# Kernel tuning notes

Measured on AMD Instinct MI355X. Metric: run time of the kernel, lower is better.

Reference implementation:

```python
import jax, jax.numpy as jnp
import numpy as np


def _bilinear_resize(x, out_h, out_w):
    """PyTorch-style bilinear resize, align_corners=False, no antialias. x: [B,C,H,W]."""
    B, C, H, W = x.shape
    sy = H / out_h
    sx = W / out_w
    ys = jnp.maximum((jnp.arange(out_h, dtype=x.dtype) + 0.5) * sy - 0.5, 0.0)
    xs = jnp.maximum((jnp.arange(out_w, dtype=x.dtype) + 0.5) * sx - 0.5, 0.0)
    y0 = jnp.minimum(jnp.floor(ys).astype(jnp.int32), H - 1)
    x0 = jnp.minimum(jnp.floor(xs).astype(jnp.int32), W - 1)
    y1 = jnp.minimum(y0 + 1, H - 1)
    x1 = jnp.minimum(x0 + 1, W - 1)
    ty = ys - y0.astype(x.dtype)  # [out_h]
    tx = xs - x0.astype(x.dtype)  # [out_w]
    row = x[:, :, y0, :] * (1.0 - ty)[None, None, :, None] + x[:, :, y1, :] * ty[None, None, :, None]
    out = row[:, :, :, x0] * (1.0 - tx)[None, None, None, :] + row[:, :, :, x1] * tx[None, None, None, :]
    return out


def setup_inputs() -> dict:
    key = jax.random.key(0)
    ks = jax.random.split(key, 6)
    T, B, Ck, Cv = 4, 4, 128, 512
    H, W, h, w = 64, 64, 32, 32
    return {
        "memory_keys": jax.random.normal(ks[0], (T, B, Ck, H, W), dtype=jnp.float32),
        "memory_values": jax.random.normal(ks[1], (T, B, Cv, H, W), dtype=jnp.float32),
        "query_value": jax.random.normal(ks[2], (B, Cv, H, W), dtype=jnp.float32),
        "memory_keys_low": jax.random.normal(ks[3], (T, B, Ck, h, w), dtype=jnp.float32),
        "memory_values_low": jax.random.normal(ks[4], (T, B, Cv, h, w), dtype=jnp.float32),
        "query_key_low": jax.random.normal(ks[5], (B, Ck, h, w), dtype=jnp.float32),
    }


def reference(memory_keys, memory_values, query_value, memory_keys_low, memory_values_low, query_key_low):
    matmul_norm = False  # init default
    T, B, Ck, h, w = memory_keys_low.shape
    H, W = memory_keys.shape[-2:]
    Cv = memory_values.shape[2]

    # ---- low-level memory read ----
    # memory_keys_low -> [B, Ck, T*h*w]
    mkl = jnp.transpose(memory_keys_low.reshape(T, B, Ck, h * w), (1, 2, 0, 3)).reshape(B, Ck, T * h * w)
    qkl = query_key_low.reshape(B, Ck, h * w)
    # key_attention: [B, T*h*w, h*w]
    key_attention = jnp.einsum('bkm,bkq->bmq', mkl, qkl)
    if matmul_norm:
        key_attention = key_attention * (Ck ** -0.5)
    key_attention = jax.nn.softmax(key_attention, axis=1)
    mvl = jnp.transpose(memory_values_low.reshape(T, B, Cv, h * w), (1, 2, 0, 3)).reshape(B, Cv, T * h * w)
    memory = jnp.einsum('bvm,bmq->bvq', mvl, key_attention).reshape(B, Cv, h, w)

    # ---- high-level channel attention ----
    g_keys = jnp.transpose(memory_keys, (1, 0, 2, 3, 4)).reshape(B, T, Ck, H * W)
    g_vals = jnp.transpose(memory_values, (1, 0, 2, 3, 4)).reshape(B, T, Cv, H * W)
    # g_attn: [B, T, Ck, Cv] = keys @ values^T over spatial dim
    g_attn = jnp.einsum('btkp,btvp->btkv', g_keys, g_vals)
    if matmul_norm:
        g_attn = g_attn * (Cv ** -0.5)
    g_attn = jax.nn.softmax(g_attn, axis=1)  # softmax over the T (frame) axis

    qv = query_value.reshape(B, Cv, H * W)
    # [B, T, Ck, H*W] -> [B, T*Ck, H, W]
    qv_out = jnp.einsum('btkv,bvq->btkq', g_attn, qv).reshape(B, T * Ck, H, W)
    qv_out = _bilinear_resize(qv_out, h, w)

    return jnp.concatenate([qv_out, memory], axis=1)  # [B, T*Ck+Cv, h, w]
```

## Files before the change

### kernel.cpp

```cpp
#include <hip/hip_runtime.h>

#define T_ 4
#define B_ 4
#define CK 128
#define CV 512
#define PP 4096
#define QQ 1024
#define MM 4096
#define NS 8

using f32x2  = __attribute__((ext_vector_type(2))) float;
using f32x4  = __attribute__((ext_vector_type(4))) float;
using bf16   = __bf16;
using bf16x2 = __attribute__((ext_vector_type(2))) __bf16;
using bf16x4 = __attribute__((ext_vector_type(4))) __bf16;
using bf16x8 = __attribute__((ext_vector_type(8))) __bf16;
using f16    = _Float16;
using f16x8  = __attribute__((ext_vector_type(8))) _Float16;

__device__ __forceinline__ f32x4 mfma16(bf16x8 a, bf16x8 b, f32x4 c) {
    return __builtin_amdgcn_mfma_f32_16x16x32_bf16(a, b, c, 0, 0, 0);
}
__device__ __forceinline__ f32x4 mfma16h(f16x8 a, f16x8 b, f32x4 c) {
    return __builtin_amdgcn_mfma_f32_16x16x32_f16(a, b, c, 0, 0, 0);
}

__device__ __forceinline__ void gload16(const void* g, void* l) {
    __builtin_amdgcn_global_load_lds(
        (const __attribute__((address_space(1))) void*)g,
        (__attribute__((address_space(3))) void*)l, 16, 0, 0);
}

__global__ __launch_bounds__(256) void k_stage1(
        const float* __restrict__ mkl, const float* __restrict__ qkl,
        bf16* __restrict__ Pt, float* __restrict__ cs_part,
        const float* __restrict__ mvl, bf16* __restrict__ Ab,
        const float* __restrict__ qv,  float* __restrict__ qvp,
        const float* __restrict__ mk,  f16* __restrict__ mkh,
        const float* __restrict__ mv,  f16* __restrict__ mvh) {
    __shared__ __align__(16) char smem[20480];
    const int bid = blockIdx.x;
    const int tid = threadIdx.x;

    if (bid % 3 == 0) {
        bf16* As = (bf16*)smem;
        bf16* Bs = (bf16*)(smem + 10240);
        bf16* Th = (bf16*)smem;

        int lb  = bid / 3;
        int sw  = (lb & 7) * 128 + (lb >> 3);
        const int b  = sw >> 8;
        const int r  = sw & 255;
        const int qy = r >> 5;
        const int mx = r & 31;
        const int m0 = mx * 128;
        const int q0 = qy * 128;
        const int t  = m0 >> 10;
        const int sm0 = m0 & 1023;

        const int lane = tid & 63;
        const int wid  = tid >> 6;
        const int wr = wid >> 1, wc = wid & 1;
        const int g = lane >> 4, li = lane & 15;

        const float* Abase = mkl + (((size_t)(t * B_ + b) * CK) << 10) + sm0;
        const float* Bbase = qkl + (((size_t)b * CK) << 10) + q0;
        const int ml   = tid & 127;
        const int half = tid >> 7;

        const f32x4 fz = {0.f, 0.f, 0.f, 0.f};
        f32x4 acc[4][4];
#pragma unroll
        for (int i = 0; i < 4; ++i)
#pragma unroll
            for (int j = 0; j < 4; ++j) acc[i][j] = fz;

        for (int k0 = 0; k0 < CK; k0 += 32) {
#pragma unroll
            for (int j = 0; j < 8; ++j) {
                int kk = 4 * j + 2 * half;
                float a0 = Abase[(k0 + kk) * 1024 + ml];
                float a1 = Abase[(k0 + kk + 1) * 1024 + ml];
                bf16x2 pa; pa.x = (bf16)a0; pa.y = (bf16)a1;
                *(bf16x2*)(As + ml * 40 + kk) = pa;
                float b0 = Bbase[(k0 + kk) * 1024 + ml];
                float b1 = Bbase[(k0 + kk + 1) * 1024 + ml];
                bf16x2 pb; pb.x = (bf16)b0; pb.y = (bf16)b1;
                *(bf16x2*)(Bs + ml * 40 + kk) = pb;
            }
            __syncthreads();
            bf16x8 af[4], bfr[4];
#pragma unroll
            for (int mf = 0; mf < 4; ++mf)
                af[mf] = *(const bf16x8*)(As + (wr * 64 + mf * 16 + li) * 40 + g * 8);
#pragma unroll
            for (int nf = 0; nf < 4; ++nf)
                bfr[nf] = *(const bf16x8*)(Bs + (wc * 64 + nf * 16 + li) * 40 + g * 8);
#pragma unroll
            for (int mf = 0; mf < 4; ++mf)
#pragma unroll
                for (int nf = 0; nf < 4; ++nf)
                    acc[mf][nf] = mfma16(af[mf], bfr[nf], acc[mf][nf]);
            __syncthreads();
        }

        float cs[4] = {0.f, 0.f, 0.f, 0.f};
        bf16x4 ebuf[4][4];
#pragma unroll
        for (int mf = 0; mf < 4; ++mf)
#pragma unroll
            for (int nf = 0; nf < 4; ++nf) {
                f32x4 v = acc[mf][nf];
                float e0 = __expf(v.x), e1 = __expf(v.y);
                float e2 = __expf(v.z), e3 = __expf(v.w);
                cs[nf] += e0 + e1 + e2 + e3;
                bf16x4 e; e.x = (bf16)e0; e.y = (bf16)e1; e.z = (bf16)e2; e.w = (bf16)e3;
                ebuf[mf][nf] = e;
            }
#pragma unroll
        for (int nf = 0; nf < 4; ++nf) {
            float s = cs[nf];
            s += __shfl_xor(s, 16);
            s += __shfl_xor(s, 32);
            if (g == 0)
                cs_part[(size_t)(((b * 32 + mx) * 2 + wr) << 10) + q0 + wc * 64 + nf * 16 + li] = s;
        }
#pragma unroll
        for (int p = 0; p < 2; ++p) {
            __syncthreads();
            if (wr == p) {
#pragma unroll
                for (int mf = 0; mf < 4; ++mf)
#pragma unroll
                    for (int nf = 0; nf < 4; ++nf) {
                        int col  = wc * 64 + nf * 16 + li;
                        int rowb = mf * 16 + g * 4;
                        *(bf16x4*)(Th + col * 72 + rowb) = ebuf[mf][nf];
                    }
            }
            __syncthreads();
#pragma unroll
            for (int pass = 0; pass < 4; ++pass) {
                int idx = pass * 256 + tid;
                int row = idx >> 3;
                int ch  = (idx & 7) * 8;
                bf16x8 v = *(const bf16x8*)(Th + row * 72 + ch);
                *(bf16x8*)(Pt + (size_t)(b * QQ + q0 + row) * MM + m0 + p * 64 + ch) = v;
            }
        }
    } else {
        int sid = bid - bid / 3 - 1;
        if (sid < 1024) {
            int base = sid * 4096 + tid;
#pragma unroll
            for (int i = 0; i < 16; ++i) {
                int idx = base + i * 256;
                f32x4 a = __builtin_nontemporal_load((const f32x4*)mv + (size_t)idx * 2);
                f32x4 c = __builtin_nontemporal_load((const f32x4*)mv + (size_t)idx * 2 + 1);
                f16x8 o;
                o[0] = (f16)a.x; o[1] = (f16)a.y; o[2] = (f16)a.z; o[3] = (f16)a.w;
                o[4] = (f16)c.x; o[5] = (f16)c.y; o[6] = (f16)c.z; o[7] = (f16)c.w;
                ((f16x8*)mvh)[idx] = o;
            }
        } else if (sid < 1280) {
            int base = (sid - 1024) * 4096 + tid;
#pragma unroll
            for (int i = 0; i < 16; ++i) {
                int idx = base + i * 256;
                f32x4 a = __builtin_nontemporal_load((const f32x4*)mk + (size_t)idx * 2);
                f32x4 c = __builtin_nontemporal_load((const f32x4*)mk + (size_t)idx * 2 + 1);
                f16x8 o;
                o[0] = (f16)a.x; o[1] = (f16)a.y; o[2] = (f16)a.z; o[3] = (f16)a.w;
                o[4] = (f16)c.x; o[5] = (f16)c.y; o[6] = (f16)c.z; o[7] = (f16)c.w;
                ((f16x8*)mkh)[idx] = o;
            }
        } else if (sid < 1536) {
            int base = (sid - 1280) * 4096 + tid;
#pragma unroll
            for (int i = 0; i < 16; ++i) {
                int idx = base + i * 256;
                f32x4 a = __builtin_nontemporal_load((const f32x4*)mvl + (size_t)idx * 2);
                f32x4 c = __builtin_nontemporal_load((const f32x4*)mvl + (size_t)idx * 2 + 1);
                bf16x8 o;
                o[0] = (bf16)a.x; o[1] = (bf16)a.y; o[2] = (bf16)a.z; o[3] = (bf16)a.w;
                o[4] = (bf16)c.x; o[5] = (bf16)c.y; o[6] = (bf16)c.z; o[7] = (bf16)c.w;
                ((bf16x8*)Ab)[idx] = o;
            }
        } else {
            int base = (sid - 1536) * 4096 + tid;
#pragma unroll
            for (int i = 0; i < 16; ++i) {
                int idx = base + i * 256;
                int q  = idx & (QQ - 1);
                int bv = idx >> 10;
                int y = q >> 5, x = q & 31;
                const float* src = qv + ((size_t)bv << 12);
                f32x2 r0 = __builtin_nontemporal_load((const f32x2*)(src + y * 128 + 2 * x));
                f32x2 r1 = __builtin_nontemporal_load((const f32x2*)(src + y * 128 + 64 + 2 * x));
                qvp[idx] = 0.25f * (r0.x + r0.y + r1.x + r1.y);
            }
        }
    }
}

__global__ __launch_bounds__(256, 2) void k_stage2(
        const f16* __restrict__ mkh, const f16* __restrict__ mvh,
        float* __restrict__ Gp,
        const bf16* __restrict__ Ab, const bf16* __restrict__ Pt,
        float* __restrict__ Mp,
        const float* __restrict__ cs_part, float* __restrict__ colsum) {
    __shared__ __align__(16) char smem[65536];
    const int bid = blockIdx.x;
    const int tid = threadIdx.x;

    if (bid < 512) {
        f16* lsA = (f16*)smem;
        f16* lsB = (f16*)(smem + 32768);

        int sw  = (bid & 7) * 64 + (bid >> 3);
        const int bt = sw >> 5;
        const int rx = sw & 31;
        const int ks = rx >> 2;
        const int v0 = (rx & 3) * 128;
        const int b = bt >> 2, t = bt & 3;

        const int lane = tid & 63;
        const int w    = tid >> 6;
        const int wr = w >> 1, wc = w & 1;
        const int g = lane >> 4, li = lane & 15;
        const int rr = lane >> 3;
        const int cg = (lane & 7) ^ rr;

        const f16* Abase = mkh + ((size_t)(t * B_ + b) * CK) * PP + ks * 512;
        const f16* Bbase = mvh + ((size_t)((t * B_ + b) * CV + v0)) * PP + ks * 512;

        auto STAGE = [&](int buf, int j) {
            int mg = j * 64;
#pragma unroll
            for (int cc = 0; cc < 4; ++cc) {
                int c = cc * 4 + w;
                int r = c * 8 + rr;
                gload16(Abase + (size_t)r * PP + mg + cg * 8, lsA + buf * 8192 + c * 512);
                gload16(Bbase + (size_t)r * PP + mg + cg * 8, lsB + buf * 8192 + c * 512);
            }
        };
        auto FRAG = [&](const f16* base, int r, int G) -> f16x8 {
            int x = r & 7;
            return *(const f16x8*)(base + (r >> 3) * 512 + x * 64 + ((G ^ x) * 8));
        };

        const f32x4 fz = {0.f, 0.f, 0.f, 0.f};
        f32x4 acc[4][4];
#pragma unroll
        for (int i = 0; i < 4; ++i)
#pragma unroll
            for (int j = 0; j < 4; ++j) acc[i][j] = fz;

        STAGE(0, 0);
        __syncthreads();
        int cur = 0;

        for (int j = 0; j < 8; ++j) {
            if (j + 1 < 8) STAGE(cur ^ 1, j + 1);
#pragma unroll
            for (int kc = 0; kc < 2; ++kc) {
                f16x8 af[4], bfr[4];
#pragma unroll
                for (int mf = 0; mf < 4; ++mf)
                    af[mf] = FRAG(lsA + cur * 8192, wr * 64 + mf * 16 + li, kc * 4 + g);
#pragma unroll
                for (int nf = 0; nf < 4; ++nf)
                    bfr[nf] = FRAG(lsB + cur * 8192, wc * 64 + nf * 16 + li, kc * 4 + g);
#pragma unroll
                for (int mf = 0; mf < 4; ++mf)
#pragma unroll
                    for (int nf = 0; nf < 4; ++nf)
                        acc[mf][nf] = mfma16h(af[mf], bfr[nf], acc[mf][nf]);
            }
            __syncthreads();
            cur ^= 1;
        }

        float* outp = Gp + (size_t)(ks * 16 + bt) * CK * CV + v0;
#pragma unroll
        for (int mf = 0; mf < 4; ++mf)
#pragma unroll
            for (int nf = 0; nf < 4; ++nf) {
                int k = wr * 64 + mf * 16 + g * 4;
                int v = wc * 64 + nf * 16 + li;
                f32x4 a = acc[mf][nf];
                outp[(size_t)(k + 0) * CV + v] = a.x;
                outp[(size_t)(k + 1) * CV + v] = a.y;
                outp[(size_t)(k + 2) * CV + v] = a.z;
                outp[(size_t)(k + 3) * CV + v] = a.w;
            }
    } else if (bid < 1024) {
        bf16* lsA = (bf16*)smem;
        bf16* lsB = (bf16*)(smem + 32768);

        int mb = bid - 512;
        int sw  = (mb & 7) * 64 + (mb >> 3);
        const int bt = sw >> 5;
        const int rx = sw & 31;
        const int q0 = (rx >> 2) * 128;
        const int v0 = (rx & 3) * 128;
        const int b = bt >> 2, t = bt & 3;

        const int lane = tid & 63;
        const int w    = tid >> 6;
        const int wr = w >> 1, wc = w & 1;
        const int g = lane >> 4, li = lane & 15;
        const int rr = lane >> 3;
        const int cg = (lane & 7) ^ rr;

        const bf16* Abase = Ab + (((size_t)((t * B_ + b) * CV + v0)) << 10);
        const bf16* Bbase = Pt + (size_t)(b * QQ + q0) * MM + t * 1024;

        auto STAGE = [&](int buf, int j) {
            int mg = j * 64;
#pragma unroll
            for (int cc = 0; cc < 4; ++cc) {
                int c = cc * 4 + w;
                int r = c * 8 + rr;
                gload16(Abase + (size_t)r * 1024 + mg + cg * 8, lsA + buf * 8192 + c * 512);
                gload16(Bbase + (size_t)r * MM   + mg + cg * 8, lsB + buf * 8192 + c * 512);
            }
        };
        auto FRAG = [&](const bf16* base, int r, int G) -> bf16x8 {
            int x = r & 7;
            return *(const bf16x8*)(base + (r >> 3) * 512 + x * 64 + ((G ^ x) * 8));
        };

        const f32x4 fz = {0.f, 0.f, 0.f, 0.f};
        f32x4 acc[4][4];
#pragma unroll
        for (int i = 0; i < 4; ++i)
#pragma unroll
            for (int j = 0; j < 4; ++j) acc[i][j] = fz;

        STAGE(0, 0);
        __syncthreads();
        int cur = 0;

        for (int j = 0; j < 16; ++j) {
            if (j + 1 < 16) STAGE(cur ^ 1, j + 1);
#pragma unroll
            for (int kc = 0; kc < 2; ++kc) {
                bf16x8 af[4], bfr[4];
#pragma unroll
                for (int mf = 0; mf < 4; ++mf)
                    af[mf] = FRAG(lsA + cur * 8192, wr * 64 + mf * 16 + li, kc * 4 + g);
#pragma unroll
                for (int nf = 0; nf < 4; ++nf)
                    bfr[nf] = FRAG(lsB + cur * 8192, wc * 64 + nf * 16 + li, kc * 4 + g);
#pragma unroll
                for (int mf = 0; mf < 4; ++mf)
#pragma unroll
                    for (int nf = 0; nf < 4; ++nf)
                        acc[mf][nf] = mfma16(af[mf], bfr[nf], acc[mf][nf]);
            }
            __syncthreads();
            cur ^= 1;
        }

#pragma unroll
        for (int nf = 0; nf < 4; ++nf) {
            int q = q0 + wc * 64 + nf * 16 + li;
#pragma unroll
            for (int mf = 0; mf < 4; ++mf) {
                int v = v0 + wr * 64 + mf * 16 + g * 4;
                f32x4 a = acc[mf][nf];
                float* base = Mp + (((size_t)bt * CV + v) << 10) + q;
                base[0 << 10] = a.x;
                base[1 << 10] = a.y;
                base[2 << 10] = a.z;
                base[3 << 10] = a.w;
            }
        }
    } else {
        int idx = (bid - 1024) * 256 + tid;
        int q = idx & (QQ - 1);
        int b = idx >> 10;
        float s = 0.f;
#pragma unroll 8
        for (int r = 0; r < 64; ++r)
            s += cs_part[(size_t)(((b * 64 + r)) << 10) + q];
        colsum[idx] = s;
    }
}

__global__ __launch_bounds__(256) void k_stage3(
        const float* __restrict__ Gp, bf16* __restrict__ Wt,
        const float* __restrict__ Mp, const float* __restrict__ colsum,
        float* __restrict__ out) {
    const int bid = blockIdx.x;
    const int tid = threadIdx.x;

    if (bid < 1024) {
        int idx = bid * 256 + tid;
        int v = idx & (CV - 1);
        int bk = idx >> 9;
        int k = bk & (CK - 1);
        int b = bk >> 7;
        float gv[4];
#pragma unroll
        for (int t = 0; t < 4; ++t) {
            float s = 0.f;
#pragma unroll
            for (int ks = 0; ks < NS; ++ks)
                s += Gp[((size_t)(ks * 16 + b * 4 + t) * CK + k) * CV + v];
            gv[t] = s;
        }
        float mx = fmaxf(fmaxf(gv[0], gv[1]), fmaxf(gv[2], gv[3]));
        float e[4], sum = 0.f;
#pragma unroll
        for (int t = 0; t < 4; ++t) { e[t] = __expf(gv[t] - mx); sum += e[t]; }
        float inv = 1.f / sum;
#pragma unroll
        for (int t = 0; t < 4; ++t)
            Wt[((size_t)((b * 4 + t) * CK + k)) * CV + v] = (bf16)(e[t] * inv);
    } else {
        int idx = ((bid - 1024) * 256 + tid) * 4;
        int q = idx & (QQ - 1);
        int v = (idx >> 10) & (CV - 1);
        int b = idx >> 19;
        f32x4 s = {0.f, 0.f, 0.f, 0.f};
#pragma unroll
        for (int t = 0; t < 4; ++t) {
            f32x4 m = *(const f32x4*)(Mp + (((size_t)((b * 4 + t) * CV + v)) << 10) + q);
            s.x += m.x; s.y += m.y; s.z += m.z; s.w += m.w;
        }
        f32x4 cs = *(const f32x4*)(colsum + (b << 10) + q);
        f32x4 o;
        o.x = s.x / cs.x; o.y = s.y / cs.y; o.z = s.z / cs.z; o.w = s.w / cs.w;
        *(f32x4*)(out + (((size_t)(b * 1024 + 512 + v)) << 10) + q) = o;
    }
}

__global__ __launch_bounds__(256) void k_qvout(const bf16* __restrict__ Wt,
                                               const float* __restrict__ QVp,
                                               float* __restrict__ out) {
    __shared__ __align__(16) char smem[27648];
    bf16* As = (bf16*)smem;
    bf16* Bs = (bf16*)(smem + 18432);

    int bid = blockIdx.x;
    int sw  = (bid & 7) * 32 + (bid >> 3);
    const int bt = sw >> 4;
    const int q0 = (sw & 15) * 64;
    const int b = bt >> 2, t = bt & 3;

    const int tid = threadIdx.x;
    const int lane = tid & 63;
    const int wid = tid >> 6;
    const int wr = wid >> 1, wc = wid & 1;
    const int g = lane >> 4, li = lane & 15;

    const bf16*  Abase = Wt + (size_t)bt * CK * CV;
    const float* Bbase = QVp + (((size_t)b * CV) << 10) + q0;

    const f32x4 fz = {0.f, 0.f, 0.f, 0.f};
    f32x4 acc[4][2];
#pragma unroll
    for (int i = 0; i < 4; ++i)
#pragma unroll
        for (int j = 0; j < 2; ++j) acc[i][j] = fz;

    const int ql  = tid & 63;
    const int grp = tid >> 6;

    for (int kk = 0; kk < 8; ++kk) {
        int vk0 = kk * 64;
#pragma unroll
        for (int pass = 0; pass < 4; ++pass) {
            int idx = pass * 256 + tid;
            int row = idx >> 3;
            int ch  = (idx & 7) * 8;
            bf16x8 v = *(const bf16x8*)(Abase + (size_t)row * CV + vk0 + ch);
            *(bf16x8*)(As + row * 72 + ch) = v;
        }
#pragma unroll
        for (int j = 0; j < 8; ++j) {
            int vv = 2 * grp + 8 * j;
            float b0 = Bbase[(size_t)(vk0 + vv) * 1024 + ql];
            float b1 = Bbase[(size_t)(vk0 + vv + 1) * 1024 + ql];
            bf16x2 p; p.x = (bf16)b0; p.y = (bf16)b1;
            *(bf16x2*)(Bs + ql * 72 + vv) = p;
        }
        __syncthreads();
#pragma unroll
        for (int kc = 0; kc < 2; ++kc) {
            bf16x8 af[4], bfr[2];
#pragma unroll
            for (int mf = 0; mf < 4; ++mf)
                af[mf] = *(const bf16x8*)(As + (wr * 64 + mf * 16 + li) * 72 + kc * 32 + g * 8);
#pragma unroll
            for (int nf = 0; nf < 2; ++nf)
                bfr[nf] = *(const bf16x8*)(Bs + (wc * 32 + nf * 16 + li) * 72 + kc * 32 + g * 8);
#pragma unroll
            for (int mf = 0; mf < 4; ++mf)
#pragma unroll
                for (int nf = 0; nf < 2; ++nf)
                    acc[mf][nf] = mfma16(af[mf], bfr[nf], acc[mf][nf]);
        }
        __syncthreads();
    }

#pragma unroll
    for (int mf = 0; mf < 4; ++mf)
#pragma unroll
        for (int nf = 0; nf < 2; ++nf) {
            int k = wr * 64 + mf * 16 + g * 4;
            int q = q0 + wc * 32 + nf * 16 + li;
            f32x4 a = acc[mf][nf];
            size_t base = ((size_t)(b * 1024 + t * 128 + k) << 10) + q;
            out[base]             = a.x;
            out[base + (1 << 10)] = a.y;
            out[base + (2 << 10)] = a.z;
            out[base + (3 << 10)] = a.w;
        }
}

extern "C" void kernel_launch(void* const* d_in, const int* in_sizes, int n_in,
                              void* d_out, int out_size, void* d_ws, size_t ws_size,
                              hipStream_t stream) {
    (void)in_sizes; (void)n_in; (void)out_size; (void)ws_size;
    const float* mk  = (const float*)d_in[0];
    const float* mv  = (const float*)d_in[1];
    const float* qv  = (const float*)d_in[2];
    const float* mkl = (const float*)d_in[3];
    const float* mvl = (const float*)d_in[4];
    const float* qkl = (const float*)d_in[5];
    float* out = (float*)d_out;

    char* w = (char*)d_ws;
    bf16*  Pt      = (bf16*)w;  w += (size_t)B_ * QQ * MM * 2;
    float* QVp     = (float*)w; w += (size_t)B_ * CV * QQ * 4;
    float* Gp      = (float*)w; w += (size_t)NS * 16 * CK * CV * 4;
    bf16*  Wt      = (bf16*)w;  w += (size_t)B_ * T_ * CK * CV * 2;
    float* colsum  = (float*)w; w += (size_t)B_ * QQ * 4;
    bf16*  Ab      = (bf16*)w;  w += (size_t)T_ * B_ * CV * QQ * 2;
    float* cs_part = (float*)w; w += (size_t)B_ * 64 * QQ * 4;
    float* Mp      = (float*)w; w += (size_t)T_ * B_ * CV * QQ * 4;
    f16*   mkh     = (f16*)w;   w += (size_t)T_ * B_ * CK * PP * 2;
    f16*   mvh     = (f16*)w;   w += (size_t)T_ * B_ * CV * PP * 2;

    k_stage1<<<dim3(3072), 256, 0, stream>>>(mkl, qkl, Pt, cs_part,
                                             mvl, Ab, qv, QVp,
                                             mk, mkh, mv, mvh);
    k_stage2<<<dim3(1040), 256, 0, stream>>>(mkh, mvh, Gp, Ab, Pt, Mp,
                                             cs_part, colsum);
    k_stage3<<<dim3(3072), 256, 0, stream>>>(Gp, Wt, Mp, colsum, out);
    k_qvout <<<dim3(256),  256, 0, stream>>>(Wt, QVp, out);
}
```

Measured before the change: 137.5 us.

## Accumulate memory-read partials atomically into output and halve channel-attention K splits

The per-frame memory-read partial buffer Mp is removed. Stage 2 now atomically adds its per-T partial products straight into the zeroed output region, and stage 3 reads and normalises them in place, which drops a large intermediate write and read. The channel-attention GEMM split count goes from 8 to 4, with longer K loops per block, so less partial data goes to Gp, and its blocks are interleaved with the memory-read blocks. Stage 1 also zeroes the output slice and vectorises the qv downsample. The cost is float atomics, which make the summation order nondeterministic and may contend, plus fewer blocks for the GEMM.

```diff
diff --git a/kernel.cpp b/kernel.cpp
--- a/kernel.cpp
+++ b/kernel.cpp
@@ -7,7 +7,7 @@
 #define PP 4096
 #define QQ 1024
 #define MM 4096
-#define NS 8
+#define NS 4
 
 using f32x2  = __attribute__((ext_vector_type(2))) float;
 using f32x4  = __attribute__((ext_vector_type(4))) float;
@@ -37,7 +37,8 @@
         const float* __restrict__ mvl, bf16* __restrict__ Ab,
         const float* __restrict__ qv,  float* __restrict__ qvp,
         const float* __restrict__ mk,  f16* __restrict__ mkh,
-        const float* __restrict__ mv,  f16* __restrict__ mvh) {
+        const float* __restrict__ mv,  f16* __restrict__ mvh,
+        float* __restrict__ out) {
     __shared__ __align__(16) char smem[20480];
     const int bid = blockIdx.x;
     const int tid = threadIdx.x;
@@ -186,18 +187,31 @@
                 o[4] = (bf16)c.x; o[5] = (bf16)c.y; o[6] = (bf16)c.z; o[7] = (bf16)c.w;
                 ((bf16x8*)Ab)[idx] = o;
             }
-        } else {
+        } else if (sid < 1792) {
             int base = (sid - 1536) * 4096 + tid;
 #pragma unroll
             for (int i = 0; i < 16; ++i) {
-                int idx = base + i * 256;
-                int q  = idx & (QQ - 1);
-                int bv = idx >> 10;
-                int y = q >> 5, x = q & 31;
-                const float* src = qv + ((size_t)bv << 12);
-                f32x2 r0 = __builtin_nontemporal_load((const f32x2*)(src + y * 128 + 2 * x));
-                f32x2 r1 = __builtin_nontemporal_load((const f32x2*)(src + y * 128 + 64 + 2 * x));
-                qvp[idx] = 0.25f * (r0.x + r0.y + r1.x + r1.y);
+                int pidx = base + i * 256;
+                int pr = pidx & 511;
+                int bv = pidx >> 9;
+                int y = pr >> 4, xp = pr & 15;
+                const float* src = qv + ((size_t)bv << 12) + y * 128 + xp * 4;
+                f32x4 r0 = __builtin_nontemporal_load((const f32x4*)src);
+                f32x4 r1 = __builtin_nontemporal_load((const f32x4*)(src + 64));
+                f32x2 o;
+                o.x = 0.25f * (r0.x + r0.y + r1.x + r1.y);
+                o.y = 0.25f * (r0.z + r0.w + r1.z + r1.w);
+                *(f32x2*)(qvp + ((size_t)bv << 10) + y * 32 + xp * 2) = o;
+            }
+        } else if (sid < 1856) {
+            int base = (sid - 1792) * 8192 + tid;
+            const f32x4 z = {0.f, 0.f, 0.f, 0.f};
+#pragma unroll
+            for (int i = 0; i < 32; ++i) {
+                int zidx = base + i * 256;
+                int b   = zidx >> 17;
+                int off = zidx & 131071;
+                ((f32x4*)out)[(size_t)b * 262144 + 131072 + off] = z;
             }
         }
     }
@@ -207,19 +221,20 @@
         const f16* __restrict__ mkh, const f16* __restrict__ mvh,
         float* __restrict__ Gp,
         const bf16* __restrict__ Ab, const bf16* __restrict__ Pt,
-        float* __restrict__ Mp,
+        float* __restrict__ out,
         const float* __restrict__ cs_part, float* __restrict__ colsum) {
     __shared__ __align__(16) char smem[65536];
     const int bid = blockIdx.x;
     const int tid = threadIdx.x;
 
-    if (bid < 512) {
+    if (bid < 768 && bid % 3 == 0) {
         f16* lsA = (f16*)smem;
         f16* lsB = (f16*)(smem + 32768);
 
-        int sw  = (bid & 7) * 64 + (bid >> 3);
-        const int bt = sw >> 5;
-        const int rx = sw & 31;
+        int gid = bid / 3;
+        int sw  = (gid & 7) * 32 + (gid >> 3);
+        const int bt = sw >> 4;
+        const int rx = sw & 15;
         const int ks = rx >> 2;
         const int v0 = (rx & 3) * 128;
         const int b = bt >> 2, t = bt & 3;
@@ -231,8 +246,8 @@
         const int rr = lane >> 3;
         const int cg = (lane & 7) ^ rr;
 
-        const f16* Abase = mkh + ((size_t)(t * B_ + b) * CK) * PP + ks * 512;
-        const f16* Bbase = mvh + ((size_t)((t * B_ + b) * CV + v0)) * PP + ks * 512;
+        const f16* Abase = mkh + ((size_t)(t * B_ + b) * CK) * PP + ks * 1024;
+        const f16* Bbase = mvh + ((size_t)((t * B_ + b) * CV + v0)) * PP + ks * 1024;
 
         auto STAGE = [&](int buf, int j) {
             int mg = j * 64;
@@ -260,8 +275,8 @@
         __syncthreads();
         int cur = 0;
 
-        for (int j = 0; j < 8; ++j) {
-            if (j + 1 < 8) STAGE(cur ^ 1, j + 1);
+        for (int j = 0; j < 16; ++j) {
+            if (j + 1 < 16) STAGE(cur ^ 1, j + 1);
 #pragma unroll
             for (int kc = 0; kc < 2; ++kc) {
                 f16x8 af[4], bfr[4];
@@ -294,11 +309,11 @@
                 outp[(size_t)(k + 2) * CV + v] = a.z;
                 outp[(size_t)(k + 3) * CV + v] = a.w;
             }
-    } else if (bid < 1024) {
+    } else if (bid < 768) {
         bf16* lsA = (bf16*)smem;
         bf16* lsB = (bf16*)(smem + 32768);
 
-        int mb = bid - 512;
+        int mb = bid - bid / 3 - 1;
         int sw  = (mb & 7) * 64 + (mb >> 3);
         const int bt = sw >> 5;
         const int rx = sw & 31;
@@ -370,15 +385,15 @@
             for (int mf = 0; mf < 4; ++mf) {
                 int v = v0 + wr * 64 + mf * 16 + g * 4;
                 f32x4 a = acc[mf][nf];
-                float* base = Mp + (((size_t)bt * CV + v) << 10) + q;
-                base[0 << 10] = a.x;
-                base[1 << 10] = a.y;
-                base[2 << 10] = a.z;
-                base[3 << 10] = a.w;
+                float* base = out + (((size_t)(b * 1024 + 512 + v)) << 10) + q;
+                atomicAdd(base,             a.x);
+                atomicAdd(base + (1 << 10), a.y);
+                atomicAdd(base + (2 << 10), a.z);
+                atomicAdd(base + (3 << 10), a.w);
             }
         }
     } else {
-        int idx = (bid - 1024) * 256 + tid;
+        int idx = (bid - 768) * 256 + tid;
         int q = idx & (QQ - 1);
         int b = idx >> 10;
         float s = 0.f;
@@ -391,8 +406,7 @@
 
 __global__ __launch_bounds__(256) void k_stage3(
         const float* __restrict__ Gp, bf16* __restrict__ Wt,
-        const float* __restrict__ Mp, const float* __restrict__ colsum,
-        float* __restrict__ out) {
+        const float* __restrict__ colsum, float* __restrict__ out) {
     const int bid = blockIdx.x;
     const int tid = threadIdx.x;
 
@@ -424,16 +438,12 @@
         int q = idx & (QQ - 1);
         int v = (idx >> 10) & (CV - 1);
         int b = idx >> 19;
-        f32x4 s = {0.f, 0.f, 0.f, 0.f};
-#pragma unroll
-        for (int t = 0; t < 4; ++t) {
-            f32x4 m = *(const f32x4*)(Mp + (((size_t)((b * 4 + t) * CV + v)) << 10) + q);
-            s.x += m.x; s.y += m.y; s.z += m.z; s.w += m.w;
-        }
+        float* p = out + (((size_t)(b * 1024 + 512 + v)) << 10) + q;
+        f32x4 s = *(f32x4*)p;
         f32x4 cs = *(const f32x4*)(colsum + (b << 10) + q);
         f32x4 o;
         o.x = s.x / cs.x; o.y = s.y / cs.y; o.z = s.z / cs.z; o.w = s.w / cs.w;
-        *(f32x4*)(out + (((size_t)(b * 1024 + 512 + v)) << 10) + q) = o;
+        *(f32x4*)p = o;
     }
 }
 
@@ -541,15 +551,14 @@
     float* colsum  = (float*)w; w += (size_t)B_ * QQ * 4;
     bf16*  Ab      = (bf16*)w;  w += (size_t)T_ * B_ * CV * QQ * 2;
     float* cs_part = (float*)w; w += (size_t)B_ * 64 * QQ * 4;
-    float* Mp      = (float*)w; w += (size_t)T_ * B_ * CV * QQ * 4;
     f16*   mkh     = (f16*)w;   w += (size_t)T_ * B_ * CK * PP * 2;
     f16*   mvh     = (f16*)w;   w += (size_t)T_ * B_ * CV * PP * 2;
 
     k_stage1<<<dim3(3072), 256, 0, stream>>>(mkl, qkl, Pt, cs_part,
                                              mvl, Ab, qv, QVp,
-                                             mk, mkh, mv, mvh);
-    k_stage2<<<dim3(1040), 256, 0, stream>>>(mkh, mvh, Gp, Ab, Pt, Mp,
+                                             mk, mkh, mv, mvh, out);
+    k_stage2<<<dim3(784),  256, 0, stream>>>(mkh, mvh, Gp, Ab, Pt, out,
                                              cs_part, colsum);
-    k_stage3<<<dim3(3072), 256, 0, stream>>>(Gp, Wt, Mp, colsum, out);
+    k_stage3<<<dim3(3072), 256, 0, stream>>>(Gp, Wt, colsum, out);
     k_qvout <<<dim3(256),  256, 0, stream>>>(Wt, QVp, out);
 }
```

Result: slower. 156.2 us (+13.6%).
